# Kernel optimization log

Hardware: AMD Instinct MI355X
Metric: run time of the kernel (lower is better)

## Reference

```python
import jax, jax.numpy as jnp
import numpy as np

WS = 21                      # window_size
K = 2 * WS + 1               # window_length = 43
SIGMA_COLOR = 1.0 / (0.1 * 0.1 * 2.0)   # 50.0
SIGMA_SPACE = 1.0 / (7.0 * 7.0 * 2.0)
LP = 0.8
C1 = 20.0
C2 = 10.0


def edge_response(im):
    """EdgeResponse (not given in snippet): Sobel gradient magnitude summed over channels -> (B,H,W)."""
    B, C, H, W = im.shape
    p = jnp.pad(im, ((0, 0), (0, 0), (1, 1), (1, 1)), mode='reflect')
    kx = jnp.array([[-1, 0, 1], [-2, 0, 2], [-1, 0, 1]], jnp.float32)
    ky = kx.T
    x = p.reshape(B * C, 1, H + 2, W + 2)
    gx = jax.lax.conv_general_dilated(x, kx[None, None], (1, 1), 'VALID').reshape(B, C, H, W)
    gy = jax.lax.conv_general_dilated(x, ky[None, None], (1, 1), 'VALID').reshape(B, C, H, W)
    return jnp.sqrt(gx * gx + gy * gy).sum(1)


def safe_pow(d, p):
    # d >= 0; forward identical to d**p (0**0.8 == 0), but avoids inf grad at d==0
    dsafe = jnp.where(d > 0, d, 1.0)
    return jnp.where(d > 0, dsafe ** p, 0.0)


def setup_inputs() -> dict:
    key = jax.random.key(0)
    k1, k2 = jax.random.split(key)
    original_images = jax.random.normal(k1, (2, 3, 128, 128), dtype=jnp.float32)
    smooth_images = jax.random.normal(k2, (2, 3, 128, 128), dtype=jnp.float32)
    return {"original_images": original_images, "smooth_images": smooth_images}


def reference(original_images, smooth_images):
    B, C, H, W = original_images.shape
    eo = edge_response(original_images)
    es = edge_response(smooth_images)
    m_large = ((eo < C1) & (es - eo > C2)).astype(jnp.float32)[:, None]  # (B,1,H,W)
    m_small = 1.0 - m_large

    pad = lambda im: jnp.pad(im, ((0, 0), (0, 0), (WS, WS), (WS, WS)), mode='reflect')
    sp = pad(smooth_images)
    op = pad(original_images)

    offs = jnp.array([(x, y) for x in range(-WS, WS + 1) for y in range(-WS, WS + 1)], jnp.int32)

    @jax.checkpoint
    def step(acc, off):
        x, y = off[0], off[1]
        s_sh = jax.lax.dynamic_slice(sp, (0, 0, WS + x, WS + y), (B, C, H, W))
        o_sh = jax.lax.dynamic_slice(op, (0, 0, WS + x, WS + y), (B, C, H, W))
        d = jnp.abs(smooth_images - s_sh)                       # |Ti - Tj|
        wr = jnp.exp(-SIGMA_COLOR * ((original_images - o_sh) ** 2).sum(1))[:, None]  # (B,1,H,W)
        xf = x.astype(jnp.float32)
        yf = y.astype(jnp.float32)
        ws_w = jnp.exp(-SIGMA_SPACE * (xf * xf + yf * yf))       # scalar spatial weight
        term = m_large * ws_w * (d * d) + m_small * wr * safe_pow(d, LP)
        return acc + term.sum(), None

    total, _ = jax.lax.scan(step, jnp.float32(0.0), offs)
    return total / (H * W * B)
```

## Files before the change

kernel.cpp:

```cpp
#include <hip/hip_runtime.h>
#include <math.h>

#define WS 21
#define KWIN 43
#define H 128
#define W 128
#define B 2
#define C 3
#define HW (H * W)
#define CHW (C * H * W)
#define NPIX (B * H * W)
#define SIGMA_SPACE (1.0f / 98.0f)
#define NSPLIT 16
#define EXT 170
#define SQ_THR_FP16 0.17f
#define NEG_SC_LOG2E 72.1347520445f
#define SG 17.509290f

typedef _Float16 h2_t __attribute__((ext_vector_type(2)));

__device__ __forceinline__ int reflect_idx(int t, int n) {
    if (t < 0) t = -t;
    if (t > n - 1) t = 2 * (n - 1) - t;
    return t;
}

__global__ __launch_bounds__(384)
void prep_kernel(const float* __restrict__ orig,
                 const float* __restrict__ smooth,
                 float* __restrict__ Gh, float* __restrict__ Qh,
                 float* __restrict__ mask, float* __restrict__ out) {
    __shared__ float row[EXT], rsq[EXT], wt[KWIN];
    const int bid = blockIdx.x;
    const int h   = bid & 127;
    const int bc  = bid >> 7;
    const int t   = threadIdx.x;
    if (bid == 0 && t == 0) out[0] = 0.f;
    if (t < KWIN) { int k = t - WS; wt[t] = __expf(-SIGMA_SPACE * (float)(k * k)); }
    const float* src = smooth + bc * HW + h * W;
    if (t < EXT) {
        float v = src[reflect_idx(t - WS, W)];
        row[t] = v; rsq[t] = v * v;
    }
    __syncthreads();
    if (t < 256) {
        const int w = t & 127;
        const float* buf = (t < 128) ? row : rsq;
        float acc = 0.f;
#pragma unroll
        for (int y = 0; y < KWIN; ++y) acc = fmaf(wt[y], buf[w + y], acc);
        ((t < 128) ? Gh : Qh)[bid * W + w] = acc;
    } else if (bc == 0 || bc == 3) {
        const int b = bc / 3;
        const int w = t - 256;
        const float* ob = orig   + b * CHW;
        const float* sb = smooth + b * CHW;
        int hm = reflect_idx(h - 1, H), hp = reflect_idx(h + 1, H);
        int wm = reflect_idx(w - 1, W), wp = reflect_idx(w + 1, W);
        float eo = 0.f, es = 0.f;
#pragma unroll
        for (int c = 0; c < C; ++c) {
            const float* po = ob + c * HW;
            const float* ps = sb + c * HW;
            {
                float a00 = po[hm * W + wm], a01 = po[hm * W + w], a02 = po[hm * W + wp];
                float a10 = po[h  * W + wm],                        a12 = po[h  * W + wp];
                float a20 = po[hp * W + wm], a21 = po[hp * W + w], a22 = po[hp * W + wp];
                float gx = (a02 - a00) + 2.f * (a12 - a10) + (a22 - a20);
                float gy = (a20 - a00) + 2.f * (a21 - a01) + (a22 - a02);
                eo += sqrtf(gx * gx + gy * gy);
            }
            {
                float a00 = ps[hm * W + wm], a01 = ps[hm * W + w], a02 = ps[hm * W + wp];
                float a10 = ps[h  * W + wm],                        a12 = ps[h  * W + wp];
                float a20 = ps[hp * W + wm], a21 = ps[hp * W + w], a22 = ps[hp * W + wp];
                float gx = (a02 - a00) + 2.f * (a12 - a10) + (a22 - a20);
                float gy = (a20 - a00) + 2.f * (a21 - a01) + (a22 - a02);
                es += sqrtf(gx * gx + gy * gy);
            }
        }
        float m = ((eo < 20.0f) && ((es - eo) > 10.0f)) ? 1.0f : 0.0f;
        mask[(b << 14) + (h << 7) + w] = m;
    }
}

__global__ __launch_bounds__(256, 4)
void smooth_loss_kernel(const float* __restrict__ orig,
                        const float* __restrict__ smooth,
                        const float* __restrict__ Gh, const float* __restrict__ Qh,
                        const float* __restrict__ mask,
                        float* __restrict__ out) {
    __shared__ uint2 se[340];
    __shared__ float red[4];

    const int t     = threadIdx.x;
    const int split = blockIdx.x & 15;
    const int rp    = (blockIdx.x >> 4) & 63;
    const int b     = blockIdx.x >> 10;
    const int h0    = rp * 2;
    const int w     = t & 127;
    const int half  = t >> 7;
    const int h     = h0 + half;
    const int lane  = t & 63;
    const int wave  = t >> 6;

    const float* ob  = orig   + b * CHW;
    const float* sb  = smooth + b * CHW;
    const float* GhB = Gh + b * 3 * HW;
    const float* QhB = Qh + b * 3 * HW;

    const int pix = (b << 14) + (h << 7) + w;
    const float m = mask[pix];
    const float thr_l = (m == 0.0f) ? SQ_THR_FP16 : -1.0f;

    float o0c, o1c, o2c, s0c, s1c, s2c;
    {
        int hw = h * W + w;
        o0c = ob[hw]; o1c = ob[HW + hw]; o2c = ob[2 * HW + hw];
        s0c = sb[hw]; s1c = sb[HW + hw]; s2c = sb[2 * HW + hw];
    }
    const h2_t c01h = { (_Float16)o0c, (_Float16)o1c };
    const h2_t c2xh = { (_Float16)o2c, (_Float16)0.f };

    const float n0 = s0c * s0c * SG, n1 = s1c * s1c * SG, n2 = s2c * s2c * SG;
    const float tc0 = -2.f * s0c, tc1 = -2.f * s1c, tc2 = -2.f * s2c;

    const int  e1r  = (t >= 170);
    const int  sc1  = reflect_idx((t - e1r * 170) - WS, W);
    const bool has2 = (t < 84);
    const int  sc2  = reflect_idx(t + 65, W);

    float accAL = 0.f, accS = 0.f;
    const int cb = half * EXT + w;

    for (int xi = split; xi < KWIN; xi += NSPLIT) {
        const int x   = xi - WS;
        const int hh0 = reflect_idx(h0 + x, H);
        const int hh1 = reflect_idx(h0 + 1 + x, H);
        const int rr  = half ? hh1 : hh0;

        __syncthreads();
        const float* pA = ob + (e1r ? hh1 : hh0) * W + sc1;
        float a0 = pA[0], a1 = pA[HW], a2 = pA[2 * HW];
        float b0 = 0.f, b1 = 0.f, b2 = 0.f;
        if (has2) {
            const float* pB = ob + hh1 * W + sc2;
            b0 = pB[0]; b1 = pB[HW]; b2 = pB[2 * HW];
        }
        const int ga = rr * W + w;
        float G0 = GhB[ga], G1 = GhB[HW + ga], G2 = GhB[2 * HW + ga];
        float Q0 = QhB[ga], Q1 = QhB[HW + ga], Q2 = QhB[2 * HW + ga];

        {
            h2_t pa01 = { (_Float16)a0, (_Float16)a1 };
            h2_t pa2x = { (_Float16)a2, (_Float16)0.f };
            se[t] = make_uint2(__builtin_bit_cast(unsigned, pa01),
                               __builtin_bit_cast(unsigned, pa2x));
            if (has2) {
                h2_t pb01 = { (_Float16)b0, (_Float16)b1 };
                h2_t pb2x = { (_Float16)b2, (_Float16)0.f };
                se[t + 256] = make_uint2(__builtin_bit_cast(unsigned, pb01),
                                         __builtin_bit_cast(unsigned, pb2x));
            }
        }

        float xf = (float)x;
        float wtx = __expf(-SIGMA_SPACE * xf * xf);
        float gsum = (n0 + fmaf(tc0, G0, Q0))
                   + (n1 + fmaf(tc1, G1, Q1))
                   + (n2 + fmaf(tc2, G2, Q2));
        accAL = fmaf(wtx, gsum, accAL);
        __syncthreads();

        unsigned mA = 0u, mB_ = 0u;
#pragma unroll
        for (int yi = 0; yi < KWIN; ++yi) {
            uint2 vv = se[cb + yi];
            h2_t a01 = __builtin_bit_cast(h2_t, vv.x);
            h2_t a2x = __builtin_bit_cast(h2_t, vv.y);
            h2_t d01 = c01h - a01;
            h2_t d2x = c2xh - a2x;
            float sq = __builtin_amdgcn_fdot2(d01, d01,
                        __builtin_amdgcn_fdot2(d2x, d2x, 0.f, false), false);
            unsigned bit = (sq < thr_l) ? 1u : 0u;
            if (yi < 21) mA  = (mA  << 1) | bit;
            else         mB_ = (mB_ << 1) | bit;
        }

        while (mA) {
            int p = __builtin_ctz(mA); mA &= mA - 1;
            int yi = 20 - p;
            int ww = reflect_idx(w + yi - WS, W);
            int a = rr * W + ww;
            float on0 = ob[a], on1 = ob[HW + a], on2 = ob[2 * HW + a];
            float sn0 = sb[a], sn1 = sb[HW + a], sn2 = sb[2 * HW + a];
            float g0 = o0c - on0, g1 = o1c - on1, g2 = o2c - on2;
            float sq = fmaf(g0, g0, fmaf(g1, g1, g2 * g2));
            float tt = -NEG_SC_LOG2E * sq;
            float d0 = fabsf(s0c - sn0), d1 = fabsf(s1c - sn1), d2 = fabsf(s2c - sn2);
            accS += __builtin_amdgcn_exp2f(fmaf(0.8f, __builtin_amdgcn_logf(d0), tt))
                  + __builtin_amdgcn_exp2f(fmaf(0.8f, __builtin_amdgcn_logf(d1), tt))
                  + __builtin_amdgcn_exp2f(fmaf(0.8f, __builtin_amdgcn_logf(d2), tt));
        }
        while (mB_) {
            int p = __builtin_ctz(mB_); mB_ &= mB_ - 1;
            int yi = 42 - p;
            int ww = reflect_idx(w + yi - WS, W);
            int a = rr * W + ww;
            float on0 = ob[a], on1 = ob[HW + a], on2 = ob[2 * HW + a];
            float sn0 = sb[a], sn1 = sb[HW + a], sn2 = sb[2 * HW + a];
            float g0 = o0c - on0, g1 = o1c - on1, g2 = o2c - on2;
            float sq = fmaf(g0, g0, fmaf(g1, g1, g2 * g2));
            float tt = -NEG_SC_LOG2E * sq;
            float d0 = fabsf(s0c - sn0), d1 = fabsf(s1c - sn1), d2 = fabsf(s2c - sn2);
            accS += __builtin_amdgcn_exp2f(fmaf(0.8f, __builtin_amdgcn_logf(d0), tt))
                  + __builtin_amdgcn_exp2f(fmaf(0.8f, __builtin_amdgcn_logf(d1), tt))
                  + __builtin_amdgcn_exp2f(fmaf(0.8f, __builtin_amdgcn_logf(d2), tt));
        }
    }

    float r = m * accAL + accS;
#pragma unroll
    for (int off = 32; off > 0; off >>= 1) r += __shfl_down(r, off, 64);
    if (lane == 0) red[wave] = r;
    __syncthreads();
    if (t == 0) atomicAdd(out, (red[0] + red[1] + red[2] + red[3]) * (1.0f / (float)NPIX));
}

extern "C" void kernel_launch(void* const* d_in, const int* in_sizes, int n_in,
                              void* d_out, int out_size, void* d_ws, size_t ws_size,
                              hipStream_t stream) {
    const float* orig   = (const float*)d_in[0];
    const float* smooth = (const float*)d_in[1];
    float* out = (float*)d_out;

    float* Gh  = (float*)d_ws;
    float* Qh  = Gh + B * C * HW;
    float* msk = Qh + B * C * HW;

    prep_kernel<<<B * C * H, 384, 0, stream>>>(orig, smooth, Gh, Qh, msk, out);
    smooth_loss_kernel<<<B * (H / 2) * NSPLIT, 256, 0, stream>>>(orig, smooth, Gh, Qh, msk, out);
}
```

Baseline: 90.00 us.

## Stage smooth image in LDS as fp16 and merge sparse-neighbor loops

Adds a second shared-memory row buffer holding the smooth image in fp16 alongside the original. The sparse pass over surviving window neighbors now reads original and smooth values from LDS instead of gathering six floats from global memory. That pass also reuses the packed fp16 dot product for the color distance, and the two bitmask loops are merged into one. The center pixel is masked out when the row offset is zero, where its contribution is zero anyway. This trades global gather latency for extra per-iteration loads and LDS stores, and lowers precision of the smooth differences and color weights to fp16.

```diff
diff --git a/kernel.cpp b/kernel.cpp
--- a/kernel.cpp
+++ b/kernel.cpp
@@ -90,7 +90,8 @@
                         const float* __restrict__ Gh, const float* __restrict__ Qh,
                         const float* __restrict__ mask,
                         float* __restrict__ out) {
-    __shared__ uint2 se[340];
+    __shared__ uint2 oA[340];
+    __shared__ uint2 sA[340];
     __shared__ float red[4];
 
     const int t     = threadIdx.x;
@@ -140,27 +141,40 @@
         const int rr  = half ? hh1 : hh0;
 
         __syncthreads();
-        const float* pA = ob + (e1r ? hh1 : hh0) * W + sc1;
-        float a0 = pA[0], a1 = pA[HW], a2 = pA[2 * HW];
-        float b0 = 0.f, b1 = 0.f, b2 = 0.f;
+        const int rowA = (e1r ? hh1 : hh0) * W;
+        const float* pAo = ob + rowA + sc1;
+        const float* pAs = sb + rowA + sc1;
+        float ao0 = pAo[0], ao1 = pAo[HW], ao2 = pAo[2 * HW];
+        float as0 = pAs[0], as1 = pAs[HW], as2 = pAs[2 * HW];
+        float bo0 = 0.f, bo1 = 0.f, bo2 = 0.f, bs0 = 0.f, bs1 = 0.f, bs2 = 0.f;
         if (has2) {
-            const float* pB = ob + hh1 * W + sc2;
-            b0 = pB[0]; b1 = pB[HW]; b2 = pB[2 * HW];
+            const float* pBo = ob + hh1 * W + sc2;
+            const float* pBs = sb + hh1 * W + sc2;
+            bo0 = pBo[0]; bo1 = pBo[HW]; bo2 = pBo[2 * HW];
+            bs0 = pBs[0]; bs1 = pBs[HW]; bs2 = pBs[2 * HW];
         }
         const int ga = rr * W + w;
         float G0 = GhB[ga], G1 = GhB[HW + ga], G2 = GhB[2 * HW + ga];
         float Q0 = QhB[ga], Q1 = QhB[HW + ga], Q2 = QhB[2 * HW + ga];
 
         {
-            h2_t pa01 = { (_Float16)a0, (_Float16)a1 };
-            h2_t pa2x = { (_Float16)a2, (_Float16)0.f };
-            se[t] = make_uint2(__builtin_bit_cast(unsigned, pa01),
-                               __builtin_bit_cast(unsigned, pa2x));
+            h2_t v01 = { (_Float16)ao0, (_Float16)ao1 };
+            h2_t v2x = { (_Float16)ao2, (_Float16)0.f };
+            oA[t] = make_uint2(__builtin_bit_cast(unsigned, v01),
+                               __builtin_bit_cast(unsigned, v2x));
+            h2_t u01 = { (_Float16)as0, (_Float16)as1 };
+            h2_t u2x = { (_Float16)as2, (_Float16)0.f };
+            sA[t] = make_uint2(__builtin_bit_cast(unsigned, u01),
+                               __builtin_bit_cast(unsigned, u2x));
             if (has2) {
-                h2_t pb01 = { (_Float16)b0, (_Float16)b1 };
-                h2_t pb2x = { (_Float16)b2, (_Float16)0.f };
-                se[t + 256] = make_uint2(__builtin_bit_cast(unsigned, pb01),
-                                         __builtin_bit_cast(unsigned, pb2x));
+                h2_t w01 = { (_Float16)bo0, (_Float16)bo1 };
+                h2_t w2x = { (_Float16)bo2, (_Float16)0.f };
+                oA[t + 256] = make_uint2(__builtin_bit_cast(unsigned, w01),
+                                         __builtin_bit_cast(unsigned, w2x));
+                h2_t y01 = { (_Float16)bs0, (_Float16)bs1 };
+                h2_t y2x = { (_Float16)bs2, (_Float16)0.f };
+                sA[t + 256] = make_uint2(__builtin_bit_cast(unsigned, y01),
+                                         __builtin_bit_cast(unsigned, y2x));
             }
         }
 
@@ -175,7 +189,7 @@
         unsigned mA = 0u, mB_ = 0u;
 #pragma unroll
         for (int yi = 0; yi < KWIN; ++yi) {
-            uint2 vv = se[cb + yi];
+            uint2 vv = oA[cb + yi];
             h2_t a01 = __builtin_bit_cast(h2_t, vv.x);
             h2_t a2x = __builtin_bit_cast(h2_t, vv.y);
             h2_t d01 = c01h - a01;
@@ -186,33 +200,27 @@
             if (yi < 21) mA  = (mA  << 1) | bit;
             else         mB_ = (mB_ << 1) | bit;
         }
-
-        while (mA) {
-            int p = __builtin_ctz(mA); mA &= mA - 1;
-            int yi = 20 - p;
-            int ww = reflect_idx(w + yi - WS, W);
-            int a = rr * W + ww;
-            float on0 = ob[a], on1 = ob[HW + a], on2 = ob[2 * HW + a];
-            float sn0 = sb[a], sn1 = sb[HW + a], sn2 = sb[2 * HW + a];
-            float g0 = o0c - on0, g1 = o1c - on1, g2 = o2c - on2;
-            float sq = fmaf(g0, g0, fmaf(g1, g1, g2 * g2));
+        if (xi == WS) mB_ &= ~(1u << 21);
+
+        unsigned mAll;
+        while ((mAll = (mA | mB_)) != 0u) {
+            int yi;
+            if (mA) { int p = __builtin_ctz(mA); mA &= mA - 1; yi = 20 - p; }
+            else    { int p = __builtin_ctz(mB_); mB_ &= mB_ - 1; yi = 42 - p; }
+            uint2 ov = oA[cb + yi];
+            uint2 sv = sA[cb + yi];
+            h2_t a01 = __builtin_bit_cast(h2_t, ov.x);
+            h2_t a2x = __builtin_bit_cast(h2_t, ov.y);
+            h2_t d01 = c01h - a01;
+            h2_t d2x = c2xh - a2x;
+            float sq = __builtin_amdgcn_fdot2(d01, d01,
+                        __builtin_amdgcn_fdot2(d2x, d2x, 0.f, false), false);
             float tt = -NEG_SC_LOG2E * sq;
-            float d0 = fabsf(s0c - sn0), d1 = fabsf(s1c - sn1), d2 = fabsf(s2c - sn2);
-            accS += __builtin_amdgcn_exp2f(fmaf(0.8f, __builtin_amdgcn_logf(d0), tt))
-                  + __builtin_amdgcn_exp2f(fmaf(0.8f, __builtin_amdgcn_logf(d1), tt))
-                  + __builtin_amdgcn_exp2f(fmaf(0.8f, __builtin_amdgcn_logf(d2), tt));
-        }
-        while (mB_) {
-            int p = __builtin_ctz(mB_); mB_ &= mB_ - 1;
-            int yi = 42 - p;
-            int ww = reflect_idx(w + yi - WS, W);
-            int a = rr * W + ww;
-            float on0 = ob[a], on1 = ob[HW + a], on2 = ob[2 * HW + a];
-            float sn0 = sb[a], sn1 = sb[HW + a], sn2 = sb[2 * HW + a];
-            float g0 = o0c - on0, g1 = o1c - on1, g2 = o2c - on2;
-            float sq = fmaf(g0, g0, fmaf(g1, g1, g2 * g2));
-            float tt = -NEG_SC_LOG2E * sq;
-            float d0 = fabsf(s0c - sn0), d1 = fabsf(s1c - sn1), d2 = fabsf(s2c - sn2);
+            h2_t u01 = __builtin_bit_cast(h2_t, sv.x);
+            h2_t u2x = __builtin_bit_cast(h2_t, sv.y);
+            float d0 = fabsf(s0c - (float)u01.x);
+            float d1 = fabsf(s1c - (float)u01.y);
+            float d2 = fabsf(s2c - (float)u2x.x);
             accS += __builtin_amdgcn_exp2f(fmaf(0.8f, __builtin_amdgcn_logf(d0), tt))
                   + __builtin_amdgcn_exp2f(fmaf(0.8f, __builtin_amdgcn_logf(d1), tt))
                   + __builtin_amdgcn_exp2f(fmaf(0.8f, __builtin_amdgcn_logf(d2), tt));
```

Result: no change. 91.51 us (+1.7%).

## Give each wave a private LDS row slice, drop block barriers, prefetch next row

Applied to the files above, without the earlier changes.

Each wavefront now handles 64 pixels of one row and stages its own 106-entry fp16 window into a private LDS slice, so the two __syncthreads per x iteration are removed. The next row's original-image values are prefetched into registers while the current row is screened. The two bit-mask loops are merged into one, and the centre pixel (x=0, y=0) is masked out explicitly. NSPLIT drops from 16 to 8, so each wave does more x iterations, with a different grid shape and occupancy.

```diff
diff --git a/kernel.cpp b/kernel.cpp
--- a/kernel.cpp
+++ b/kernel.cpp
@@ -11,11 +11,11 @@
 #define CHW (C * H * W)
 #define NPIX (B * H * W)
 #define SIGMA_SPACE (1.0f / 98.0f)
-#define NSPLIT 16
-#define EXT 170
+#define NSPLIT 8
 #define SQ_THR_FP16 0.17f
 #define NEG_SC_LOG2E 72.1347520445f
 #define SG 17.509290f
+#define WSLOTS 108
 
 typedef _Float16 h2_t __attribute__((ext_vector_type(2)));
 
@@ -30,7 +30,7 @@
                  const float* __restrict__ smooth,
                  float* __restrict__ Gh, float* __restrict__ Qh,
                  float* __restrict__ mask, float* __restrict__ out) {
-    __shared__ float row[EXT], rsq[EXT], wt[KWIN];
+    __shared__ float row[170], rsq[170], wt[KWIN];
     const int bid = blockIdx.x;
     const int h   = bid & 127;
     const int bc  = bid >> 7;
@@ -38,7 +38,7 @@
     if (bid == 0 && t == 0) out[0] = 0.f;
     if (t < KWIN) { int k = t - WS; wt[t] = __expf(-SIGMA_SPACE * (float)(k * k)); }
     const float* src = smooth + bc * HW + h * W;
-    if (t < EXT) {
+    if (t < 170) {
         float v = src[reflect_idx(t - WS, W)];
         row[t] = v; rsq[t] = v * v;
     }
@@ -84,25 +84,26 @@
     }
 }
 
-__global__ __launch_bounds__(256, 4)
-void smooth_loss_kernel(const float* __restrict__ orig,
-                        const float* __restrict__ smooth,
-                        const float* __restrict__ Gh, const float* __restrict__ Qh,
-                        const float* __restrict__ mask,
-                        float* __restrict__ out) {
-    __shared__ uint2 se[340];
+__global__ __launch_bounds__(256)
+void screen_kernel(const float* __restrict__ orig,
+                   const float* __restrict__ smooth,
+                   const float* __restrict__ Gh, const float* __restrict__ Qh,
+                   const float* __restrict__ mask,
+                   float* __restrict__ out) {
+    __shared__ uint2 oA[4 * WSLOTS];
     __shared__ float red[4];
 
-    const int t     = threadIdx.x;
-    const int split = blockIdx.x & 15;
-    const int rp    = (blockIdx.x >> 4) & 63;
-    const int b     = blockIdx.x >> 10;
-    const int h0    = rp * 2;
-    const int w     = t & 127;
-    const int half  = t >> 7;
-    const int h     = h0 + half;
-    const int lane  = t & 63;
-    const int wave  = t >> 6;
+    const int t    = threadIdx.x;
+    const int wave = t >> 6;
+    const int lane = t & 63;
+    const int gw   = blockIdx.x * 4 + wave;
+    const int split = gw & 7;
+    const int half  = (gw >> 3) & 1;
+    const int h     = (gw >> 4) & 127;
+    const int b     = gw >> 11;
+    const int w0    = half * 64;
+    const int w     = w0 + lane;
+    const int wb    = wave * WSLOTS;
 
     const float* ob  = orig   + b * CHW;
     const float* sb  = smooth + b * CHW;
@@ -125,71 +126,77 @@
     const float n0 = s0c * s0c * SG, n1 = s1c * s1c * SG, n2 = s2c * s2c * SG;
     const float tc0 = -2.f * s0c, tc1 = -2.f * s1c, tc2 = -2.f * s2c;
 
-    const int  e1r  = (t >= 170);
-    const int  sc1  = reflect_idx((t - e1r * 170) - WS, W);
-    const bool has2 = (t < 84);
-    const int  sc2  = reflect_idx(t + 65, W);
+    const int  sc1  = reflect_idx(w0 - WS + lane, W);
+    const bool has2 = (lane < 42);
+    const int  sc2  = reflect_idx(w0 + 43 + lane, W);
 
     float accAL = 0.f, accS = 0.f;
-    const int cb = half * EXT + w;
+
+    float a0, a1, a2, b0 = 0.f, b1 = 0.f, b2 = 0.f;
+    {
+        const int rr0 = reflect_idx(h + split - WS, H);
+        const float* prow = ob + rr0 * W;
+        a0 = prow[sc1]; a1 = prow[HW + sc1]; a2 = prow[2 * HW + sc1];
+        if (has2) { b0 = prow[sc2]; b1 = prow[HW + sc2]; b2 = prow[2 * HW + sc2]; }
+    }
 
     for (int xi = split; xi < KWIN; xi += NSPLIT) {
-        const int x   = xi - WS;
-        const int hh0 = reflect_idx(h0 + x, H);
-        const int hh1 = reflect_idx(h0 + 1 + x, H);
-        const int rr  = half ? hh1 : hh0;
-
-        __syncthreads();
-        const float* pA = ob + (e1r ? hh1 : hh0) * W + sc1;
-        float a0 = pA[0], a1 = pA[HW], a2 = pA[2 * HW];
-        float b0 = 0.f, b1 = 0.f, b2 = 0.f;
-        if (has2) {
-            const float* pB = ob + hh1 * W + sc2;
-            b0 = pB[0]; b1 = pB[HW]; b2 = pB[2 * HW];
-        }
-        const int ga = rr * W + w;
-        float G0 = GhB[ga], G1 = GhB[HW + ga], G2 = GhB[2 * HW + ga];
-        float Q0 = QhB[ga], Q1 = QhB[HW + ga], Q2 = QhB[2 * HW + ga];
+        const int x  = xi - WS;
+        const int rr = reflect_idx(h + x, H);
 
         {
-            h2_t pa01 = { (_Float16)a0, (_Float16)a1 };
-            h2_t pa2x = { (_Float16)a2, (_Float16)0.f };
-            se[t] = make_uint2(__builtin_bit_cast(unsigned, pa01),
-                               __builtin_bit_cast(unsigned, pa2x));
+            h2_t v01 = { (_Float16)a0, (_Float16)a1 };
+            h2_t v2x = { (_Float16)a2, (_Float16)0.f };
+            oA[wb + lane] = make_uint2(__builtin_bit_cast(unsigned, v01),
+                                       __builtin_bit_cast(unsigned, v2x));
             if (has2) {
-                h2_t pb01 = { (_Float16)b0, (_Float16)b1 };
-                h2_t pb2x = { (_Float16)b2, (_Float16)0.f };
-                se[t + 256] = make_uint2(__builtin_bit_cast(unsigned, pb01),
-                                         __builtin_bit_cast(unsigned, pb2x));
+                h2_t u01 = { (_Float16)b0, (_Float16)b1 };
+                h2_t u2x = { (_Float16)b2, (_Float16)0.f };
+                oA[wb + 64 + lane] = make_uint2(__builtin_bit_cast(unsigned, u01),
+                                                __builtin_bit_cast(unsigned, u2x));
             }
         }
 
-        float xf = (float)x;
-        float wtx = __expf(-SIGMA_SPACE * xf * xf);
-        float gsum = (n0 + fmaf(tc0, G0, Q0))
-                   + (n1 + fmaf(tc1, G1, Q1))
-                   + (n2 + fmaf(tc2, G2, Q2));
-        accAL = fmaf(wtx, gsum, accAL);
-        __syncthreads();
+        const int xin = xi + NSPLIT;
+        if (xin < KWIN) {
+            const int rrn = reflect_idx(h + xin - WS, H);
+            const float* prow = ob + rrn * W;
+            a0 = prow[sc1]; a1 = prow[HW + sc1]; a2 = prow[2 * HW + sc1];
+            if (has2) { b0 = prow[sc2]; b1 = prow[HW + sc2]; b2 = prow[2 * HW + sc2]; }
+        }
+
+        {
+            const int ga = rr * W + w;
+            float G0 = GhB[ga], G1 = GhB[HW + ga], G2 = GhB[2 * HW + ga];
+            float Q0 = QhB[ga], Q1 = QhB[HW + ga], Q2 = QhB[2 * HW + ga];
+            float xf = (float)x;
+            float wtx = __expf(-SIGMA_SPACE * xf * xf);
+            float gsum = (n0 + fmaf(tc0, G0, Q0))
+                       + (n1 + fmaf(tc1, G1, Q1))
+                       + (n2 + fmaf(tc2, G2, Q2));
+            accAL = fmaf(wtx, gsum, accAL);
+        }
 
         unsigned mA = 0u, mB_ = 0u;
 #pragma unroll
         for (int yi = 0; yi < KWIN; ++yi) {
-            uint2 vv = se[cb + yi];
-            h2_t a01 = __builtin_bit_cast(h2_t, vv.x);
-            h2_t a2x = __builtin_bit_cast(h2_t, vv.y);
-            h2_t d01 = c01h - a01;
-            h2_t d2x = c2xh - a2x;
+            uint2 vv = oA[wb + lane + yi];
+            h2_t p01 = __builtin_bit_cast(h2_t, vv.x);
+            h2_t p2x = __builtin_bit_cast(h2_t, vv.y);
+            h2_t d01 = c01h - p01;
+            h2_t d2x = c2xh - p2x;
             float sq = __builtin_amdgcn_fdot2(d01, d01,
                         __builtin_amdgcn_fdot2(d2x, d2x, 0.f, false), false);
             unsigned bit = (sq < thr_l) ? 1u : 0u;
             if (yi < 21) mA  = (mA  << 1) | bit;
             else         mB_ = (mB_ << 1) | bit;
         }
-
-        while (mA) {
-            int p = __builtin_ctz(mA); mA &= mA - 1;
-            int yi = 20 - p;
+        if (xi == WS) mB_ &= ~(1u << 21);
+
+        while (mA | mB_) {
+            int yi;
+            if (mA) { int p = __builtin_ctz(mA); mA &= mA - 1; yi = 20 - p; }
+            else    { int p = __builtin_ctz(mB_); mB_ &= mB_ - 1; yi = 42 - p; }
             int ww = reflect_idx(w + yi - WS, W);
             int a = rr * W + ww;
             float on0 = ob[a], on1 = ob[HW + a], on2 = ob[2 * HW + a];
@@ -202,21 +209,6 @@
                   + __builtin_amdgcn_exp2f(fmaf(0.8f, __builtin_amdgcn_logf(d1), tt))
                   + __builtin_amdgcn_exp2f(fmaf(0.8f, __builtin_amdgcn_logf(d2), tt));
         }
-        while (mB_) {
-            int p = __builtin_ctz(mB_); mB_ &= mB_ - 1;
-            int yi = 42 - p;
-            int ww = reflect_idx(w + yi - WS, W);
-            int a = rr * W + ww;
-            float on0 = ob[a], on1 = ob[HW + a], on2 = ob[2 * HW + a];
-            float sn0 = sb[a], sn1 = sb[HW + a], sn2 = sb[2 * HW + a];
-            float g0 = o0c - on0, g1 = o1c - on1, g2 = o2c - on2;
-            float sq = fmaf(g0, g0, fmaf(g1, g1, g2 * g2));
-            float tt = -NEG_SC_LOG2E * sq;
-            float d0 = fabsf(s0c - sn0), d1 = fabsf(s1c - sn1), d2 = fabsf(s2c - sn2);
-            accS += __builtin_amdgcn_exp2f(fmaf(0.8f, __builtin_amdgcn_logf(d0), tt))
-                  + __builtin_amdgcn_exp2f(fmaf(0.8f, __builtin_amdgcn_logf(d1), tt))
-                  + __builtin_amdgcn_exp2f(fmaf(0.8f, __builtin_amdgcn_logf(d2), tt));
-        }
     }
 
     float r = m * accAL + accS;
@@ -239,5 +231,5 @@
     float* msk = Qh + B * C * HW;
 
     prep_kernel<<<B * C * H, 384, 0, stream>>>(orig, smooth, Gh, Qh, msk, out);
-    smooth_loss_kernel<<<B * (H / 2) * NSPLIT, 256, 0, stream>>>(orig, smooth, Gh, Qh, msk, out);
-}
+    screen_kernel<<<(B * H * 2 * NSPLIT) / 4, 256, 0, stream>>>(orig, smooth, Gh, Qh, msk, out);
+}
```

Result: faster. 87.64 us (-2.6%).
